# Kernel tuning notes

Measured on AMD Instinct MI355X. Metric: run time of the kernel, lower is better.

Reference implementation:

```python
import jax, jax.numpy as jnp
import numpy as np

L_COORD = 5.0
L_NOOBJ = 0.5


def _iou(box, tbox):
    """IoU of center-format boxes (cx, cy, w, h); broadcasts over leading dims."""
    ax1 = box[..., 0] - box[..., 2] / 2
    ay1 = box[..., 1] - box[..., 3] / 2
    ax2 = box[..., 0] + box[..., 2] / 2
    ay2 = box[..., 1] + box[..., 3] / 2
    bx1 = tbox[..., 0] - tbox[..., 2] / 2
    by1 = tbox[..., 1] - tbox[..., 3] / 2
    bx2 = tbox[..., 0] + tbox[..., 2] / 2
    by2 = tbox[..., 1] + tbox[..., 3] / 2
    iw = jnp.maximum(jnp.minimum(ax2, bx2) - jnp.maximum(ax1, bx1), 0.0)
    ih = jnp.maximum(jnp.minimum(ay2, by2) - jnp.maximum(ay1, by1), 0.0)
    inter = iw * ih
    union = box[..., 2] * box[..., 3] + tbox[..., 2] * tbox[..., 3] - inter
    return inter / jnp.maximum(union, 1e-10)


def setup_inputs() -> dict:
    key = jax.random.key(0)
    k1, k2, k3 = jax.random.split(key, 3)
    B, S, C = 16384, 7, 30
    pred = jax.random.uniform(k1, (B, S, S, C), dtype=jnp.float32)
    target = jax.random.uniform(k2, (B, S, S, C), dtype=jnp.float32)
    obj = (jax.random.uniform(k3, (B, S, S)) > 0.8).astype(jnp.float32)
    target = target.at[..., 4].set(obj)
    target = target.at[..., 9].set(obj)
    return {"pred": pred, "target": target}


def reference(pred, target):
    B = pred.shape[0]
    objf = (target[..., 4] == 1.0).astype(pred.dtype)   # [B,7,7]
    noobjf = 1.0 - objf

    # two predicted boxes per cell: [B,7,7,2,5]
    pboxes = pred[..., :10].reshape(pred.shape[:3] + (2, 5))
    tbox = target[..., :4]                               # [B,7,7,4] (box1 of target, as in the loop)

    # IoU of both predicted boxes vs the target box; detached as in the original
    iou = jax.lax.stop_gradient(_iou(pboxes[..., :4], tbox[..., None, :]))  # [B,7,7,2]
    # original tie-break: iou1 > iou2 -> box 0, else box 1
    best = jnp.where(iou[..., 0] > iou[..., 1], 0, 1)    # [B,7,7]
    sel = jax.nn.one_hot(best, 2, dtype=pred.dtype)      # responder mask [B,7,7,2]
    wbox = jnp.einsum('bijk,bijkc->bijc', sel, pboxes)   # responder box [B,7,7,5]
    wiou = jnp.max(iou, axis=-1)                         # winner IoU = new conf target

    # localization loss (sum over object cells)
    xy = jnp.sum((wbox[..., :2] - tbox[..., :2]) ** 2, axis=-1)
    wh = jnp.sum((jnp.sqrt(wbox[..., 2:4]) - jnp.sqrt(tbox[..., 2:4])) ** 2, axis=-1)
    loc_loss = jnp.sum((xy + wh) * objf)

    # responder confidence loss vs (detached) IoU
    conf_loss_obj = jnp.sum(((wbox[..., 4] - wiou) ** 2) * objf)

    # class cross-entropy, mean over object cells (nn.CrossEntropyLoss default)
    logp = jax.nn.log_softmax(pred[..., 10:30], axis=-1)
    cls_t = jnp.argmax(target[..., 10:30], axis=-1)
    ce = -jnp.take_along_axis(logp, cls_t[..., None], axis=-1)[..., 0]
    n_obj = jnp.maximum(jnp.sum(objf), 1.0)
    cls_loss = jnp.sum(ce * objf) / n_obj

    # no-object confidence loss on both box slots (channels 4 and 9)
    conf_loss_no_obj = jnp.sum(((pred[..., 4] - target[..., 4]) ** 2 +
                                (pred[..., 9] - target[..., 9]) ** 2) * noobjf)

    total = (L_COORD * loc_loss + conf_loss_obj +
             L_NOOBJ * conf_loss_no_obj + cls_loss) / B
    return total, loc_loss, conf_loss_obj, conf_loss_no_obj, cls_loss
```

## Files before the change

kernel.cpp:

```cpp
#include <hip/hip_runtime.h>
#include <stdint.h>

#define L_COORD 5.0f
#define L_NOOBJ 0.5f

#define BLOCK 128
#define CPB   128
#define CHUNK_FLOATS (CPB * 30)
#define KB_PER_TENSOR 15

__device__ __forceinline__ void cell_terms(const float* __restrict__ p,
                                           const float* __restrict__ t,
                                           float& loc, float& cobj, float& cnoobj,
                                           float& clsn, float& nobj)
{
    float objf = (t[4] == 1.0f) ? 1.0f : 0.0f;
    float noobjf = 1.0f - objf;

    float tx1 = t[0] - t[2] * 0.5f, ty1 = t[1] - t[3] * 0.5f;
    float tx2 = t[0] + t[2] * 0.5f, ty2 = t[1] + t[3] * 0.5f;
    float tarea = t[2] * t[3];

    float a0x1 = p[0] - p[2] * 0.5f, a0y1 = p[1] - p[3] * 0.5f;
    float a0x2 = p[0] + p[2] * 0.5f, a0y2 = p[1] + p[3] * 0.5f;
    float iw0 = fmaxf(fminf(a0x2, tx2) - fmaxf(a0x1, tx1), 0.0f);
    float ih0 = fmaxf(fminf(a0y2, ty2) - fmaxf(a0y1, ty1), 0.0f);
    float in0 = iw0 * ih0;
    float iou0 = in0 / fmaxf(p[2] * p[3] + tarea - in0, 1e-10f);

    float a1x1 = p[5] - p[7] * 0.5f, a1y1 = p[6] - p[8] * 0.5f;
    float a1x2 = p[5] + p[7] * 0.5f, a1y2 = p[6] + p[8] * 0.5f;
    float iw1 = fmaxf(fminf(a1x2, tx2) - fmaxf(a1x1, tx1), 0.0f);
    float ih1 = fmaxf(fminf(a1y2, ty2) - fmaxf(a1y1, ty1), 0.0f);
    float in1 = iw1 * ih1;
    float iou1 = in1 / fmaxf(p[7] * p[8] + tarea - in1, 1e-10f);

    bool b0 = iou0 > iou1;
    float wx  = b0 ? p[0] : p[5];
    float wy  = b0 ? p[1] : p[6];
    float ww  = b0 ? p[2] : p[7];
    float whh = b0 ? p[3] : p[8];
    float wc  = b0 ? p[4] : p[9];
    float wiou = fmaxf(iou0, iou1);

    float dx = wx - t[0], dy = wy - t[1];
    float xy = dx * dx + dy * dy;
    float dw = sqrtf(ww) - sqrtf(t[2]);
    float dh = sqrtf(whh) - sqrtf(t[3]);
    float wh = dw * dw + dh * dh;
    loc += (xy + wh) * objf;

    float dc = wc - wiou;
    cobj += dc * dc * objf;

    float m = p[10];
#pragma unroll
    for (int k = 11; k < 30; ++k) m = fmaxf(m, p[k]);
    float s = 0.0f;
#pragma unroll
    for (int k = 10; k < 30; ++k) s += __expf(p[k] - m);

    float tm = t[10];
    float psel = p[10];
#pragma unroll
    for (int k = 11; k < 30; ++k) {
        bool gt = t[k] > tm;
        tm = gt ? t[k] : tm;
        psel = gt ? p[k] : psel;
    }
    float ce = (m + __logf(s)) - psel;
    clsn += ce * objf;
    nobj += objf;

    float d4 = p[4] - t[4], d9 = p[9] - t[9];
    cnoobj += (d4 * d4 + d9 * d9) * noobjf;
}

__global__ __launch_bounds__(BLOCK) void yolo_loss_partial(
    const float* __restrict__ pred, const float* __restrict__ target,
    float* __restrict__ partial,
    int nchunks)
{
    __shared__ float smp[CHUNK_FLOATS];
    __shared__ float smt[CHUNK_FLOATS];

    const int wid  = threadIdx.x >> 6;
    const int lane = threadIdx.x & 63;

    float loc = 0.0f, cobj = 0.0f, cnoobj = 0.0f, clsn = 0.0f, nobj = 0.0f;

    const float* sbase = wid ? target : pred;
    float* dbase = wid ? smt : smp;

    for (int chunk = blockIdx.x; chunk < nchunks; chunk += gridDim.x) {
        const size_t fbase = (size_t)chunk * CHUNK_FLOATS;

        {
            const float* src = sbase + fbase + lane * 4;
#pragma unroll
            for (int c = 0; c < KB_PER_TENSOR; ++c)
                __builtin_amdgcn_global_load_lds(
                    (const __attribute__((address_space(1))) void*)(src + c * 256),
                    (__attribute__((address_space(3))) void*)(dbase + c * 256), 16, 0, 0);
        }
        asm volatile("s_waitcnt vmcnt(0)" ::: "memory");
        __syncthreads();

        {
            const float2* p2 = reinterpret_cast<const float2*>(&smp[threadIdx.x * 30]);
            const float2* t2 = reinterpret_cast<const float2*>(&smt[threadIdx.x * 30]);
            float p[30], t[30];
#pragma unroll
            for (int k = 0; k < 15; ++k) {
                float2 v = p2[k];
                p[2 * k] = v.x; p[2 * k + 1] = v.y;
            }
#pragma unroll
            for (int k = 0; k < 15; ++k) {
                float2 v = t2[k];
                t[2 * k] = v.x; t[2 * k + 1] = v.y;
            }
            cell_terms(p, t, loc, cobj, cnoobj, clsn, nobj);
        }

        __syncthreads();
    }

#pragma unroll
    for (int off = 32; off > 0; off >>= 1) {
        loc    += __shfl_down(loc, off);
        cobj   += __shfl_down(cobj, off);
        cnoobj += __shfl_down(cnoobj, off);
        clsn   += __shfl_down(clsn, off);
        nobj   += __shfl_down(nobj, off);
    }

    __shared__ float sm[2][5];
    if (lane == 0) {
        sm[wid][0] = loc; sm[wid][1] = cobj; sm[wid][2] = cnoobj;
        sm[wid][3] = clsn; sm[wid][4] = nobj;
    }
    __syncthreads();
    if (threadIdx.x == 0) {
        int g = gridDim.x, b = blockIdx.x;
        partial[0 * g + b] = sm[0][0] + sm[1][0];
        partial[1 * g + b] = sm[0][1] + sm[1][1];
        partial[2 * g + b] = sm[0][2] + sm[1][2];
        partial[3 * g + b] = sm[0][3] + sm[1][3];
        partial[4 * g + b] = sm[0][4] + sm[1][4];
    }
}

__global__ __launch_bounds__(256) void yolo_reduce(
    const float* __restrict__ partial, int n, float* __restrict__ out, float invB)
{
    float v0 = 0.f, v1 = 0.f, v2 = 0.f, v3 = 0.f, v4 = 0.f;
    for (int i = threadIdx.x; i < n; i += 256) {
        v0 += partial[0 * n + i];
        v1 += partial[1 * n + i];
        v2 += partial[2 * n + i];
        v3 += partial[3 * n + i];
        v4 += partial[4 * n + i];
    }
#pragma unroll
    for (int off = 32; off > 0; off >>= 1) {
        v0 += __shfl_down(v0, off);
        v1 += __shfl_down(v1, off);
        v2 += __shfl_down(v2, off);
        v3 += __shfl_down(v3, off);
        v4 += __shfl_down(v4, off);
    }
    __shared__ float sm[4][5];
    int lane = threadIdx.x & 63;
    int wid = threadIdx.x >> 6;
    if (lane == 0) {
        sm[wid][0] = v0; sm[wid][1] = v1; sm[wid][2] = v2;
        sm[wid][3] = v3; sm[wid][4] = v4;
    }
    __syncthreads();
    if (threadIdx.x == 0) {
        float loc = 0.f, cobj = 0.f, cnoobj = 0.f, clsum = 0.f, nobj = 0.f;
#pragma unroll
        for (int w = 0; w < 4; ++w) {
            loc += sm[w][0]; cobj += sm[w][1]; cnoobj += sm[w][2];
            clsum += sm[w][3]; nobj += sm[w][4];
        }
        float nn = fmaxf(nobj, 1.0f);
        float cls = clsum / nn;
        float total = (L_COORD * loc + cobj + L_NOOBJ * cnoobj + cls) * invB;
        out[0] = total;
        out[1] = loc;
        out[2] = cobj;
        out[3] = cnoobj;
        out[4] = cls;
    }
}

extern "C" void kernel_launch(void* const* d_in, const int* in_sizes, int n_in,
                              void* d_out, int out_size, void* d_ws, size_t ws_size,
                              hipStream_t stream) {
    const float* pred = (const float*)d_in[0];
    const float* target = (const float*)d_in[1];
    float* out = (float*)d_out;
    float* partial = (float*)d_ws;

    int ncells = in_sizes[0] / 30;
    int B = ncells / 49;
    int nchunks = ncells / CPB;

    int blocks = nchunks;
    int maxb = (int)(ws_size / (5 * sizeof(float)));
    if (blocks > maxb) blocks = maxb;
    if (blocks < 1) blocks = 1;

    yolo_loss_partial<<<blocks, BLOCK, 0, stream>>>(pred, target, partial, nchunks);
    yolo_reduce<<<1, 256, 0, stream>>>(partial, blocks, out, 1.0f / (float)B);
}
```

Before: 44.41 us.

## Use 256-thread blocks and a persistent grid of 512 blocks

```diff
diff --git a/kernel.cpp b/kernel.cpp
--- a/kernel.cpp
+++ b/kernel.cpp
@@ -4,10 +4,10 @@
 #define L_COORD 5.0f
 #define L_NOOBJ 0.5f
 
-#define BLOCK 128
-#define CPB   128
+#define BLOCK 256
+#define CPB   256
 #define CHUNK_FLOATS (CPB * 30)
-#define KB_PER_TENSOR 15
+#define PERSIST_BLOCKS 512
 
 __device__ __forceinline__ void cell_terms(const float* __restrict__ p,
                                            const float* __restrict__ t,
@@ -87,22 +87,20 @@
     const int wid  = threadIdx.x >> 6;
     const int lane = threadIdx.x & 63;
 
+    const float* sbase = (wid & 2) ? target : pred;
+    float* dbase       = ((wid & 2) ? smt : smp) + (wid & 1) * 15 * 256;
+    const int sub0     = (wid & 1) * 15;
+
     float loc = 0.0f, cobj = 0.0f, cnoobj = 0.0f, clsn = 0.0f, nobj = 0.0f;
 
-    const float* sbase = wid ? target : pred;
-    float* dbase = wid ? smt : smp;
-
     for (int chunk = blockIdx.x; chunk < nchunks; chunk += gridDim.x) {
-        const size_t fbase = (size_t)chunk * CHUNK_FLOATS;
-
-        {
-            const float* src = sbase + fbase + lane * 4;
-#pragma unroll
-            for (int c = 0; c < KB_PER_TENSOR; ++c)
-                __builtin_amdgcn_global_load_lds(
-                    (const __attribute__((address_space(1))) void*)(src + c * 256),
-                    (__attribute__((address_space(3))) void*)(dbase + c * 256), 16, 0, 0);
-        }
+        const float* src = sbase + (size_t)chunk * CHUNK_FLOATS + sub0 * 256 + lane * 4;
+#pragma unroll
+        for (int c = 0; c < 15; ++c)
+            __builtin_amdgcn_global_load_lds(
+                (const __attribute__((address_space(1))) void*)(src + c * 256),
+                (__attribute__((address_space(3))) void*)(dbase + c * 256), 16, 0, 0);
+
         asm volatile("s_waitcnt vmcnt(0)" ::: "memory");
         __syncthreads();
 
@@ -135,19 +133,25 @@
         nobj   += __shfl_down(nobj, off);
     }
 
-    __shared__ float sm[2][5];
+    __shared__ float sm[4][5];
     if (lane == 0) {
         sm[wid][0] = loc; sm[wid][1] = cobj; sm[wid][2] = cnoobj;
         sm[wid][3] = clsn; sm[wid][4] = nobj;
     }
     __syncthreads();
     if (threadIdx.x == 0) {
+        float a0 = 0.f, a1 = 0.f, a2 = 0.f, a3 = 0.f, a4 = 0.f;
+#pragma unroll
+        for (int w = 0; w < 4; ++w) {
+            a0 += sm[w][0]; a1 += sm[w][1]; a2 += sm[w][2];
+            a3 += sm[w][3]; a4 += sm[w][4];
+        }
         int g = gridDim.x, b = blockIdx.x;
-        partial[0 * g + b] = sm[0][0] + sm[1][0];
-        partial[1 * g + b] = sm[0][1] + sm[1][1];
-        partial[2 * g + b] = sm[0][2] + sm[1][2];
-        partial[3 * g + b] = sm[0][3] + sm[1][3];
-        partial[4 * g + b] = sm[0][4] + sm[1][4];
+        partial[0 * g + b] = a0;
+        partial[1 * g + b] = a1;
+        partial[2 * g + b] = a2;
+        partial[3 * g + b] = a3;
+        partial[4 * g + b] = a4;
     }
 }
 
@@ -208,7 +212,7 @@
     int B = ncells / 49;
     int nchunks = ncells / CPB;
 
-    int blocks = nchunks;
+    int blocks = nchunks < PERSIST_BLOCKS ? nchunks : PERSIST_BLOCKS;
     int maxb = (int)(ws_size / (5 * sizeof(float)));
     if (blocks > maxb) blocks = maxb;
     if (blocks < 1) blocks = 1;
```

New measurement: 38.44 us, median of 2. 13.5% less time.

## Double-buffer LDS loads in a persistent grid-stride loop

Applied to the files above, without the earlier changes.

```diff
diff --git a/kernel.cpp b/kernel.cpp
--- a/kernel.cpp
+++ b/kernel.cpp
@@ -7,7 +7,7 @@
 #define BLOCK 128
 #define CPB   128
 #define CHUNK_FLOATS (CPB * 30)
-#define KB_PER_TENSOR 15
+#define PERSIST_BLOCKS 512
 
 __device__ __forceinline__ void cell_terms(const float* __restrict__ p,
                                            const float* __restrict__ t,
@@ -81,34 +81,49 @@
     float* __restrict__ partial,
     int nchunks)
 {
-    __shared__ float smp[CHUNK_FLOATS];
-    __shared__ float smt[CHUNK_FLOATS];
+    __shared__ float lds[2][2][CHUNK_FLOATS];
 
     const int wid  = threadIdx.x >> 6;
     const int lane = threadIdx.x & 63;
+    const int G    = gridDim.x;
+
+    const float* sbase = wid ? target : pred;
 
     float loc = 0.0f, cobj = 0.0f, cnoobj = 0.0f, clsn = 0.0f, nobj = 0.0f;
 
-    const float* sbase = wid ? target : pred;
-    float* dbase = wid ? smt : smp;
-
-    for (int chunk = blockIdx.x; chunk < nchunks; chunk += gridDim.x) {
-        const size_t fbase = (size_t)chunk * CHUNK_FLOATS;
-
-        {
-            const float* src = sbase + fbase + lane * 4;
-#pragma unroll
-            for (int c = 0; c < KB_PER_TENSOR; ++c)
+    int chunk = blockIdx.x;
+    int cur = 0;
+
+    if (chunk < nchunks) {
+        const float* src = sbase + (size_t)chunk * CHUNK_FLOATS + lane * 4;
+        float* dst = &lds[0][wid][0];
+#pragma unroll
+        for (int c = 0; c < 15; ++c)
+            __builtin_amdgcn_global_load_lds(
+                (const __attribute__((address_space(1))) void*)(src + c * 256),
+                (__attribute__((address_space(3))) void*)(dst + c * 256), 16, 0, 0);
+    }
+
+    for (; chunk < nchunks; chunk += G) {
+        int next = chunk + G;
+        if (next < nchunks) {
+            const float* src = sbase + (size_t)next * CHUNK_FLOATS + lane * 4;
+            float* dst = &lds[cur ^ 1][wid][0];
+#pragma unroll
+            for (int c = 0; c < 15; ++c)
                 __builtin_amdgcn_global_load_lds(
                     (const __attribute__((address_space(1))) void*)(src + c * 256),
-                    (__attribute__((address_space(3))) void*)(dbase + c * 256), 16, 0, 0);
+                    (__attribute__((address_space(3))) void*)(dst + c * 256), 16, 0, 0);
+            asm volatile("s_waitcnt vmcnt(15)" ::: "memory");
+        } else {
+            asm volatile("s_waitcnt vmcnt(0)" ::: "memory");
         }
-        asm volatile("s_waitcnt vmcnt(0)" ::: "memory");
-        __syncthreads();
+        __builtin_amdgcn_s_barrier();
+        __builtin_amdgcn_sched_barrier(0);
 
         {
-            const float2* p2 = reinterpret_cast<const float2*>(&smp[threadIdx.x * 30]);
-            const float2* t2 = reinterpret_cast<const float2*>(&smt[threadIdx.x * 30]);
+            const float2* p2 = reinterpret_cast<const float2*>(&lds[cur][0][threadIdx.x * 30]);
+            const float2* t2 = reinterpret_cast<const float2*>(&lds[cur][1][threadIdx.x * 30]);
             float p[30], t[30];
 #pragma unroll
             for (int k = 0; k < 15; ++k) {
@@ -123,7 +138,9 @@
             cell_terms(p, t, loc, cobj, cnoobj, clsn, nobj);
         }
 
-        __syncthreads();
+        __builtin_amdgcn_sched_barrier(0);
+        __builtin_amdgcn_s_barrier();
+        cur ^= 1;
     }
 
 #pragma unroll
@@ -208,7 +225,7 @@
     int B = ncells / 49;
     int nchunks = ncells / CPB;
 
-    int blocks = nchunks;
+    int blocks = nchunks < PERSIST_BLOCKS ? nchunks : PERSIST_BLOCKS;
     int maxb = (int)(ws_size / (5 * sizeof(float)));
     if (blocks > maxb) blocks = maxb;
     if (blocks < 1) blocks = 1;
```

New measurement: 39.02 us. -12.1%, faster.
